# Kernel optimization log

Hardware: AMD Instinct MI355X
Metric: run time of the kernel (lower is better)

## Reference

```python
import jax, jax.numpy as jnp
import numpy as np

N = 8            # n_qubits
N_LAYERS_CRZ = 1

_H = jnp.array([[1.0, 1.0], [1.0, -1.0]], dtype=jnp.complex64) / np.sqrt(2).astype(np.float32)
_X2 = jnp.array([[0.0, 1.0], [1.0, 0.0]], dtype=jnp.complex64)
_I2 = jnp.eye(2, dtype=jnp.complex64)


def _apply_1q(state, U, q):
    # shared (2,2) gate on wire q; state: (B, 2,...,2)
    moved = jnp.moveaxis(state, 1 + q, -1)
    out = jnp.einsum('ij,...j->...i', U, moved)
    return jnp.moveaxis(out, -1, 1 + q)


def _apply_1q_batched(state, U, q):
    # per-sample (B,2,2) gate on wire q
    moved = jnp.moveaxis(state, 1 + q, -1)
    out = jnp.einsum('bij,b...j->b...i', U, moved)
    return jnp.moveaxis(out, -1, 1 + q)


def _apply_diag_batched(state, d, q):
    # per-sample diagonal (B,2) phases on wire q
    shape = (d.shape[0],) + (1,) * q + (2,) + (1,) * (N - 1 - q)
    return state * d.reshape(shape)


def _apply_ctrl_diag(state, ph, c, t):
    # controlled diagonal: apply phases ph (2,) on target t when control c == 1
    moved = jnp.moveaxis(state, (1 + c, 1 + t), (-2, -1))
    d = jnp.stack([jnp.ones(2, state.dtype), ph])  # (bc, bt)
    moved = moved * d
    return jnp.moveaxis(moved, (-2, -1), (1 + c, 1 + t))


def _apply_ctrl(state, U, c, t):
    # controlled (2,2) gate, control c, target t
    moved = jnp.moveaxis(state, (1 + c, 1 + t), (-2, -1))
    s0 = moved[..., 0, :]
    s1 = jnp.einsum('ij,...j->...i', U, moved[..., 1, :])
    out = jnp.stack([s0, s1], axis=-2)
    return jnp.moveaxis(out, (-2, -1), (1 + c, 1 + t))


def _circuit(X, weights):
    B = X.shape[0]
    state = jnp.zeros((B,) + (2,) * N, jnp.complex64)
    state = state.at[(slice(None),) + (0,) * N].set(1.0)

    # encoding: H, RZ(x[2q]), RY(x[2q+1]) on each wire q (2q+1 < 16 always)
    for q in range(N):
        state = _apply_1q(state, _H, q)
        th_z = X[:, 2 * q]
        d = jnp.stack([jnp.exp(-0.5j * th_z), jnp.exp(0.5j * th_z)], axis=-1)  # (B,2)
        state = _apply_diag_batched(state, d, q)
        half = 0.5 * X[:, 2 * q + 1]
        c, s = jnp.cos(half), jnp.sin(half)
        Ury = jnp.stack([jnp.stack([c, -s], -1), jnp.stack([s, c], -1)], -2)  # (B,2,2) real
        state = _apply_1q_batched(state, Ury, q)

    # CRZ ring
    for l in range(N_LAYERS_CRZ):
        for i in range(N):
            th = weights[l, i]
            ph = jnp.stack([jnp.exp(-0.5j * th), jnp.exp(0.5j * th)])
            state = _apply_ctrl_diag(state, ph, i, (i + 1) % N)

    # all-to-all CRX
    for i in range(N):
        for j in range(N):
            if j == i:
                continue
            half = 0.5 * weights[N_LAYERS_CRZ + i, j]
            Urx = jnp.cos(half) * _I2 + (-1j * jnp.sin(half)) * _X2
            state = _apply_ctrl(state, Urx, i, j)

    probs = jnp.real(state * jnp.conj(state)).reshape(B, 2 ** N)
    q_idx = jnp.arange(N)
    bits = (jnp.arange(2 ** N)[None, :] >> (N - 1 - q_idx)[:, None]) & 1  # (N, 2^N)
    signs = (1.0 - 2.0 * bits).astype(probs.dtype)
    return probs @ signs.T  # (B, N) <Z_q> expectations


def setup_inputs() -> dict:
    key = jax.random.key(0)
    k1, k2 = jax.random.split(key)
    X = jax.random.normal(k1, (16384, 2 * N), dtype=jnp.float32)
    weights = jax.random.normal(k2, (N_LAYERS_CRZ + N, (N_LAYERS_CRZ + N) * N), dtype=jnp.float32)
    return {"X": X, "weights": weights}


def reference(X, weights):
    return _circuit(X, weights)
```

## Files before the change

### kernel.cpp

```cpp
#include <hip/hip_runtime.h>


typedef _Float16 half_t;
typedef __attribute__((ext_vector_type(8))) _Float16 half8;
typedef __attribute__((ext_vector_type(4))) float float4v;

static __device__ __forceinline__ float rlane(float v, int src) {
    return __int_as_float(__builtin_amdgcn_readlane(__float_as_int(v), src));
}
template <int CTRL>
static __device__ __forceinline__ float dppf(float x) {
    return __int_as_float(__builtin_amdgcn_update_dpp(0, __float_as_int(x), CTRL, 0xF, 0xF, true));
}
static __device__ __forceinline__ float xor1f(float x) { return dppf<0xB1>(x); }
static __device__ __forceinline__ float xor2f(float x) { return dppf<0x4E>(x); }
static __device__ __forceinline__ float xor4f(float x) { return dppf<0x1B>(dppf<0x141>(x)); }
static __device__ __forceinline__ float xor8f(float x) { return dppf<0x128>(x); }
static __device__ __forceinline__ float xorMf(float x, int m) {
    if (m == 1) return xor1f(x);
    if (m == 2) return xor2f(x);
    if (m == 4) return xor4f(x);
    return xor8f(x);
}
static __device__ __forceinline__ float2 xorM2(float2 a, int m) {
    float2 t; t.x = xorMf(a.x, m); t.y = xorMf(a.y, m); return t;
}
static __device__ __forceinline__ float2 cmul(float2 a, float2 b) {
    float2 t;
    t.x = a.x * b.x - a.y * b.y;
    t.y = a.x * b.y + a.y * b.x;
    return t;
}
static __device__ __forceinline__ float2 rotA(float2 t, float2 u, float c, float s) {
    float2 d;
    d.x = c * t.x + s * u.y;
    d.y = c * t.y - s * u.x;
    return d;
}

__global__ __launch_bounds__(256, 4) void buildV_kernel(const float* __restrict__ W,
                                                        half_t* __restrict__ Vr,
                                                        half_t* __restrict__ Vi) {
    const int lane = threadIdx.x & 63;
    const int g = lane >> 4;
    const int s = lane & 15;
    const int eid = (blockIdx.x * 4 + (threadIdx.x >> 6)) * 4 + g;

    float gcv = 1.0f, gsv = 0.0f;
    if (lane < 56) {
        const int i = lane / 7;
        const int jj = lane - 7 * i;
        const int j = jj + (jj >= i ? 1 : 0);
        const float h = 0.5f * W[(1 + i) * 72 + j];
        __sincosf(h, &gsv, &gcv);
    }

    float2 a[16];
#pragma unroll
    for (int r = 0; r < 16; ++r) {
        a[r].x = (s == (eid & 15) && r == (eid >> 4)) ? 1.0f : 0.0f;
        a[r].y = 0.0f;
    }

    {
        const float wv0 = W[0], wv1 = W[1], wv2 = W[2], wv3 = W[3];
        const float wv4 = W[4], wv5 = W[5], wv6 = W[6], wv7 = W[7];
        const int s3 = (s >> 3) & 1, s2 = (s >> 2) & 1, s1 = (s >> 1) & 1, s0 = s & 1;
        float phiS = 0.0f;
        phiS += s3 ? (s2 ? wv4 : -wv4) : 0.0f;
        phiS += s2 ? (s1 ? wv5 : -wv5) : 0.0f;
        phiS += s1 ? (s0 ? wv6 : -wv6) : 0.0f;
        const float termA = s3 ? wv3 : -wv3;
        const float termB = s0 ? wv7 : 0.0f;
#pragma unroll
        for (int r = 0; r < 16; ++r) {
            const int b3 = (r >> 3) & 1, b2 = (r >> 2) & 1, b1 = (r >> 1) & 1, b0 = r & 1;
            float phi = phiS + (b3 ? termB : -termB);
            if (b3) phi += b2 ? wv0 : -wv0;
            if (b2) phi += b1 ? wv1 : -wv1;
            if (b1) phi += b0 ? wv2 : -wv2;
            if (b0) phi += termA;
            float2 ph;
            __sincosf(0.5f * phi, &ph.y, &ph.x);
            a[r] = cmul(a[r], ph);
        }
    }

#pragma unroll
    for (int i = 0; i < 4; ++i) {
        float cg[8], sg[8];
#pragma unroll
        for (int j = 0; j < 8; ++j) {
            if (j == i) continue;
            const int gi = i * 7 + (j < i ? j : j - 1);
            cg[j] = rlane(gcv, gi);
            sg[j] = rlane(gsv, gi);
        }
        const int rc = 3 - i;
#pragma unroll
        for (int j = 0; j < 8; ++j) {
            if (j == i) continue;
            if (j < 4) {
                const int mt = 1 << (3 - j);
#pragma unroll
                for (int r = 0; r < 16; ++r) {
                    if (!((r >> rc) & 1)) continue;
                    if (r & mt) continue;
                    const int rp = r | mt;
                    const float2 t = a[r], u = a[rp];
                    a[r]  = rotA(t, u, cg[j], sg[j]);
                    a[rp] = rotA(u, t, cg[j], sg[j]);
                }
            } else {
                const int ms = 1 << (7 - j);
#pragma unroll
                for (int r = 0; r < 16; ++r) {
                    if (!((r >> rc) & 1)) continue;
                    const float2 p = xorM2(a[r], ms);
                    a[r] = rotA(a[r], p, cg[j], sg[j]);
                }
            }
        }
    }

#pragma unroll
    for (int k = 1; k <= 8; k <<= 1) {
        const bool sk = (s & k) != 0;
#pragma unroll
        for (int r = 0; r < 16; ++r) {
            if (r & k) continue;
            const int rp = r | k;
            const float2 tp = xorM2(a[rp], k);
            const float2 tr = xorM2(a[r],  k);
            a[r].x  = sk ? tp.x : a[r].x;
            a[r].y  = sk ? tp.y : a[r].y;
            a[rp].x = sk ? a[rp].x : tr.x;
            a[rp].y = sk ? a[rp].y : tr.y;
        }
    }

#pragma unroll
    for (int i = 4; i < 8; ++i) {
        float cg[8], sg[8];
#pragma unroll
        for (int j = 0; j < 8; ++j) {
            if (j == i) continue;
            const int gi = i * 7 + (j < i ? j : j - 1);
            cg[j] = rlane(gcv, gi);
            sg[j] = rlane(gsv, gi);
        }
        const int rc = 7 - i;
#pragma unroll
        for (int j = 0; j < 8; ++j) {
            if (j == i) continue;
            if (j < 4) {
                const int ms = 1 << (3 - j);
#pragma unroll
                for (int r = 0; r < 16; ++r) {
                    if (!((r >> rc) & 1)) continue;
                    const float2 p = xorM2(a[r], ms);
                    a[r] = rotA(a[r], p, cg[j], sg[j]);
                }
            } else {
                const int mt = 1 << (7 - j);
#pragma unroll
                for (int r = 0; r < 16; ++r) {
                    if (!((r >> rc) & 1)) continue;
                    if (r & mt) continue;
                    const int rp = r | mt;
                    const float2 t = a[r], u = a[rp];
                    a[r]  = rotA(t, u, cg[j], sg[j]);
                    a[rp] = rotA(u, t, cg[j], sg[j]);
                }
            }
        }
    }

    const int ks = eid >> 5, kq = (eid >> 3) & 3, jj = eid & 7;
#pragma unroll
    for (int r = 0; r < 16; ++r) {
        const int off = ((s * 8 + ks) * 64 + kq * 16 + r) * 8 + jj;
        Vr[off] = (half_t)a[r].x;
        Vi[off] = (half_t)a[r].y;
    }
}

#define PSI_STRIDE 264

__global__ __launch_bounds__(256, 2) void gemm_kernel(const float* __restrict__ X,
                                                      const half_t* __restrict__ Vr,
                                                      const half_t* __restrict__ Vi,
                                                      float* __restrict__ out,
                                                      int B) {
    __shared__ float4 u_lds[32][8];
    __shared__ half_t psir[32][PSI_STRIDE];
    __shared__ half_t psii[32][PSI_STRIDE];
    __shared__ float part[32][8][4];

    const int tid = threadIdx.x;
    const int rowbase = blockIdx.x * 32;

    {
        const int m = tid >> 3, q = tid & 7;
        int row = rowbase + m; if (row >= B) row = B - 1;
        const float2 xq = ((const float2*)X)[row * 8 + q];
        float cz, sz, cy, sy;
        __sincosf(0.5f * xq.x, &sz, &cz);
        __sincosf(0.5f * xq.y, &sy, &cy);
        float4 u;
        u.x = (cy - sy) * cz;  u.y = -(cy + sy) * sz;
        u.z = (cy + sy) * cz;  u.w = (cy - sy) * sz;
        u_lds[m][q] = u;
    }
    __syncthreads();

    {
        const int m = tid >> 3, kh = tid & 7;
        float2 uu[8][2];
#pragma unroll
        for (int q = 0; q < 8; ++q) {
            const float4 u = u_lds[m][q];
            uu[q][0].x = u.x; uu[q][0].y = u.y;
            uu[q][1].x = u.z; uu[q][1].y = u.w;
        }
        const float2 pre = cmul(cmul(uu[0][(kh >> 2) & 1], uu[1][(kh >> 1) & 1]), uu[2][kh & 1]);
        float2 t1[2], t2[4], t3[8], t4[16];
        t1[0] = cmul(pre, uu[3][0]);  t1[1] = cmul(pre, uu[3][1]);
#pragma unroll
        for (int h = 0; h < 2; ++h) { t2[2*h] = cmul(t1[h], uu[4][0]); t2[2*h+1] = cmul(t1[h], uu[4][1]); }
#pragma unroll
        for (int h = 0; h < 4; ++h) { t3[2*h] = cmul(t2[h], uu[5][0]); t3[2*h+1] = cmul(t2[h], uu[5][1]); }
#pragma unroll
        for (int h = 0; h < 8; ++h) { t4[2*h] = cmul(t3[h], uu[6][0]); t4[2*h+1] = cmul(t3[h], uu[6][1]); }
        unsigned int* pr = (unsigned int*)&psir[m][kh * 32];
        unsigned int* pi = (unsigned int*)&psii[m][kh * 32];
#pragma unroll
        for (int h = 0; h < 16; ++h) {
            const float2 v0 = cmul(t4[h], uu[7][0]);
            const float2 v1 = cmul(t4[h], uu[7][1]);
            union { half_t h2[2]; unsigned int u; } cr, ci;
            cr.h2[0] = (half_t)v0.x; cr.h2[1] = (half_t)v1.x;
            ci.h2[0] = (half_t)v0.y; ci.h2[1] = (half_t)v1.y;
            pr[h] = cr.u; pi[h] = ci.u;
        }
    }
    __syncthreads();

    const int w = tid >> 6;
    const int lane = tid & 63;
    const int m16 = lane & 15;
    float4v Cr[2][4], Ci[2][4];
#pragma unroll
    for (int rt = 0; rt < 2; ++rt)
#pragma unroll
        for (int t = 0; t < 4; ++t) {
            Cr[rt][t] = (float4v){0.f, 0.f, 0.f, 0.f};
            Ci[rt][t] = (float4v){0.f, 0.f, 0.f, 0.f};
        }
#pragma unroll
    for (int ks = 0; ks < 8; ++ks) {
        const int koff = ks * 32 + (lane >> 4) * 8;
        const half8 Ar0 = *(const half8*)&psir[m16][koff];
        const half8 Ai0 = *(const half8*)&psii[m16][koff];
        const half8 Ar1 = *(const half8*)&psir[16 + m16][koff];
        const half8 Ai1 = *(const half8*)&psii[16 + m16][koff];
#pragma unroll
        for (int t = 0; t < 4; ++t) {
            const int T = w * 4 + t;
            const int boff = ((T * 8 + ks) * 64 + lane) * 8;
            const half8 Br = *(const half8*)(Vr + boff);
            const half8 Bi = *(const half8*)(Vi + boff);
            const half8 Bin = -Bi;
            Cr[0][t] = __builtin_amdgcn_mfma_f32_16x16x32_f16(Ar0, Br,  Cr[0][t], 0, 0, 0);
            Cr[0][t] = __builtin_amdgcn_mfma_f32_16x16x32_f16(Ai0, Bin, Cr[0][t], 0, 0, 0);
            Ci[0][t] = __builtin_amdgcn_mfma_f32_16x16x32_f16(Ar0, Bi,  Ci[0][t], 0, 0, 0);
            Ci[0][t] = __builtin_amdgcn_mfma_f32_16x16x32_f16(Ai0, Br,  Ci[0][t], 0, 0, 0);
            Cr[1][t] = __builtin_amdgcn_mfma_f32_16x16x32_f16(Ar1, Br,  Cr[1][t], 0, 0, 0);
            Cr[1][t] = __builtin_amdgcn_mfma_f32_16x16x32_f16(Ai1, Bin, Cr[1][t], 0, 0, 0);
            Ci[1][t] = __builtin_amdgcn_mfma_f32_16x16x32_f16(Ar1, Bi,  Ci[1][t], 0, 0, 0);
            Ci[1][t] = __builtin_amdgcn_mfma_f32_16x16x32_f16(Ai1, Br,  Ci[1][t], 0, 0, 0);
        }
    }

    const float sw0 = ((w >> 1) & 1) ? -1.0f : 1.0f;
    const float sw1 = (w & 1) ? -1.0f : 1.0f;
    const int quad = lane >> 4;
#pragma unroll
    for (int rt = 0; rt < 2; ++rt) {
        float A0[4] = {0.f, 0.f, 0.f, 0.f};
        float A2[4] = {0.f, 0.f, 0.f, 0.f};
        float A3[4] = {0.f, 0.f, 0.f, 0.f};
#pragma unroll
        for (int t = 0; t < 4; ++t) {
            const int T = w * 4 + t;
            const float s2 = ((T >> 1) & 1) ? -1.0f : 1.0f;
            const float s3 = (T & 1) ? -1.0f : 1.0f;
#pragma unroll
            for (int reg = 0; reg < 4; ++reg) {
                const float cr = Cr[rt][t][reg], ci = Ci[rt][t][reg];
                const float P = cr * cr + ci * ci;
                A0[reg] += P;
                A2[reg] += s2 * P;
                A3[reg] += s3 * P;
            }
        }
#pragma unroll
        for (int reg = 0; reg < 4; ++reg) {
            float Z = A0[reg], E7, E6, E5, E4;
            { const float tt = xor1f(Z); E7 = Z - tt; Z += tt; }
            { const float tt = xor2f(Z); E6 = Z - tt; Z += tt; E7 += xor2f(E7); }
            { const float tt = xor4f(Z); E5 = Z - tt; Z += tt; E7 += xor4f(E7); E6 += xor4f(E6); }
            { const float tt = xor8f(Z); E4 = Z - tt; Z += tt; E7 += xor8f(E7); E6 += xor8f(E6); E5 += xor8f(E5); }
            float Q2 = A2[reg]; Q2 += xor1f(Q2); Q2 += xor2f(Q2); Q2 += xor4f(Q2); Q2 += xor8f(Q2);
            float Q3 = A3[reg]; Q3 += xor1f(Q3); Q3 += xor2f(Q3); Q3 += xor4f(Q3); Q3 += xor8f(Q3);
            if (m16 == 0) {
                const int m = rt * 16 + quad * 4 + reg;
                part[m][0][w] = sw0 * Z;
                part[m][1][w] = sw1 * Z;
                part[m][2][w] = Q2;
                part[m][3][w] = Q3;
                part[m][4][w] = E4;
                part[m][5][w] = E5;
                part[m][6][w] = E6;
                part[m][7][w] = E7;
            }
        }
    }
    __syncthreads();
    {
        const int m = tid >> 3, q = tid & 7;
        const int row = rowbase + m;
        if (row < B) {
            const float v = part[m][q][0] + part[m][q][1] + part[m][q][2] + part[m][q][3];
            out[row * 8 + q] = v * (1.0f / 256.0f);
        }
    }
}

extern "C" void kernel_launch(void* const* d_in, const int* in_sizes, int n_in,
                              void* d_out, int out_size, void* d_ws, size_t ws_size,
                              hipStream_t stream) {
    const float* X = (const float*)d_in[0];
    const float* W = (const float*)d_in[1];
    float* out = (float*)d_out;
    const int B = in_sizes[0] / 16;
    half_t* Vr = (half_t*)d_ws;
    half_t* Vi = Vr + 256 * 256;
    buildV_kernel<<<16, 256, 0, stream>>>(W, Vr, Vi);
    gemm_kernel<<<(B + 31) / 32, 256, 0, stream>>>(X, Vr, Vi, out, B);
}
```

Before: 81.53 us.

## Fuse unitary build and GEMM into one kernel with a grid-wide atomic barrier

Merges the separate unitary-construction kernel and the batched GEMM kernel into one launch. The first 16 blocks build V and publish it with a threadfence, while all blocks prepare their per-row product states in LDS; then every block waits on a global atomic counter before reading V for the MFMA stage. The aim is to remove the inter-kernel gap and overlap V construction with the state preparation. In exchange it adds a memset launch for the counter and a spin barrier that relies on all 512 blocks being co-resident, which risks deadlock if occupancy drops. The order of two independent MFMA calls also changes.

```diff
diff --git a/kernel.cpp b/kernel.cpp
--- a/kernel.cpp
+++ b/kernel.cpp
@@ -38,167 +38,168 @@
     return d;
 }
 
-__global__ __launch_bounds__(256, 4) void buildV_kernel(const float* __restrict__ W,
-                                                        half_t* __restrict__ Vr,
-                                                        half_t* __restrict__ Vi) {
-    const int lane = threadIdx.x & 63;
-    const int g = lane >> 4;
-    const int s = lane & 15;
-    const int eid = (blockIdx.x * 4 + (threadIdx.x >> 6)) * 4 + g;
-
-    float gcv = 1.0f, gsv = 0.0f;
-    if (lane < 56) {
-        const int i = lane / 7;
-        const int jj = lane - 7 * i;
-        const int j = jj + (jj >= i ? 1 : 0);
-        const float h = 0.5f * W[(1 + i) * 72 + j];
-        __sincosf(h, &gsv, &gcv);
-    }
-
-    float2 a[16];
-#pragma unroll
-    for (int r = 0; r < 16; ++r) {
-        a[r].x = (s == (eid & 15) && r == (eid >> 4)) ? 1.0f : 0.0f;
-        a[r].y = 0.0f;
-    }
-
-    {
-        const float wv0 = W[0], wv1 = W[1], wv2 = W[2], wv3 = W[3];
-        const float wv4 = W[4], wv5 = W[5], wv6 = W[6], wv7 = W[7];
-        const int s3 = (s >> 3) & 1, s2 = (s >> 2) & 1, s1 = (s >> 1) & 1, s0 = s & 1;
-        float phiS = 0.0f;
-        phiS += s3 ? (s2 ? wv4 : -wv4) : 0.0f;
-        phiS += s2 ? (s1 ? wv5 : -wv5) : 0.0f;
-        phiS += s1 ? (s0 ? wv6 : -wv6) : 0.0f;
-        const float termA = s3 ? wv3 : -wv3;
-        const float termB = s0 ? wv7 : 0.0f;
-#pragma unroll
-        for (int r = 0; r < 16; ++r) {
-            const int b3 = (r >> 3) & 1, b2 = (r >> 2) & 1, b1 = (r >> 1) & 1, b0 = r & 1;
-            float phi = phiS + (b3 ? termB : -termB);
-            if (b3) phi += b2 ? wv0 : -wv0;
-            if (b2) phi += b1 ? wv1 : -wv1;
-            if (b1) phi += b0 ? wv2 : -wv2;
-            if (b0) phi += termA;
-            float2 ph;
-            __sincosf(0.5f * phi, &ph.y, &ph.x);
-            a[r] = cmul(a[r], ph);
-        }
-    }
-
-#pragma unroll
-    for (int i = 0; i < 4; ++i) {
-        float cg[8], sg[8];
-#pragma unroll
-        for (int j = 0; j < 8; ++j) {
-            if (j == i) continue;
-            const int gi = i * 7 + (j < i ? j : j - 1);
-            cg[j] = rlane(gcv, gi);
-            sg[j] = rlane(gsv, gi);
-        }
-        const int rc = 3 - i;
-#pragma unroll
-        for (int j = 0; j < 8; ++j) {
-            if (j == i) continue;
-            if (j < 4) {
-                const int mt = 1 << (3 - j);
-#pragma unroll
-                for (int r = 0; r < 16; ++r) {
-                    if (!((r >> rc) & 1)) continue;
-                    if (r & mt) continue;
-                    const int rp = r | mt;
-                    const float2 t = a[r], u = a[rp];
-                    a[r]  = rotA(t, u, cg[j], sg[j]);
-                    a[rp] = rotA(u, t, cg[j], sg[j]);
-                }
-            } else {
-                const int ms = 1 << (7 - j);
-#pragma unroll
-                for (int r = 0; r < 16; ++r) {
-                    if (!((r >> rc) & 1)) continue;
-                    const float2 p = xorM2(a[r], ms);
-                    a[r] = rotA(a[r], p, cg[j], sg[j]);
-                }
-            }
-        }
-    }
-
-#pragma unroll
-    for (int k = 1; k <= 8; k <<= 1) {
-        const bool sk = (s & k) != 0;
-#pragma unroll
-        for (int r = 0; r < 16; ++r) {
-            if (r & k) continue;
-            const int rp = r | k;
-            const float2 tp = xorM2(a[rp], k);
-            const float2 tr = xorM2(a[r],  k);
-            a[r].x  = sk ? tp.x : a[r].x;
-            a[r].y  = sk ? tp.y : a[r].y;
-            a[rp].x = sk ? a[rp].x : tr.x;
-            a[rp].y = sk ? a[rp].y : tr.y;
-        }
-    }
-
-#pragma unroll
-    for (int i = 4; i < 8; ++i) {
-        float cg[8], sg[8];
-#pragma unroll
-        for (int j = 0; j < 8; ++j) {
-            if (j == i) continue;
-            const int gi = i * 7 + (j < i ? j : j - 1);
-            cg[j] = rlane(gcv, gi);
-            sg[j] = rlane(gsv, gi);
-        }
-        const int rc = 7 - i;
-#pragma unroll
-        for (int j = 0; j < 8; ++j) {
-            if (j == i) continue;
-            if (j < 4) {
-                const int ms = 1 << (3 - j);
-#pragma unroll
-                for (int r = 0; r < 16; ++r) {
-                    if (!((r >> rc) & 1)) continue;
-                    const float2 p = xorM2(a[r], ms);
-                    a[r] = rotA(a[r], p, cg[j], sg[j]);
-                }
-            } else {
-                const int mt = 1 << (7 - j);
-#pragma unroll
-                for (int r = 0; r < 16; ++r) {
-                    if (!((r >> rc) & 1)) continue;
-                    if (r & mt) continue;
-                    const int rp = r | mt;
-                    const float2 t = a[r], u = a[rp];
-                    a[r]  = rotA(t, u, cg[j], sg[j]);
-                    a[rp] = rotA(u, t, cg[j], sg[j]);
-                }
-            }
-        }
-    }
-
-    const int ks = eid >> 5, kq = (eid >> 3) & 3, jj = eid & 7;
-#pragma unroll
-    for (int r = 0; r < 16; ++r) {
-        const int off = ((s * 8 + ks) * 64 + kq * 16 + r) * 8 + jj;
-        Vr[off] = (half_t)a[r].x;
-        Vi[off] = (half_t)a[r].y;
-    }
-}
-
 #define PSI_STRIDE 264
 
-__global__ __launch_bounds__(256, 2) void gemm_kernel(const float* __restrict__ X,
-                                                      const half_t* __restrict__ Vr,
-                                                      const half_t* __restrict__ Vi,
-                                                      float* __restrict__ out,
-                                                      int B) {
+__global__ __launch_bounds__(256, 2) void fused_kernel(const float* __restrict__ X,
+                                                       const float* __restrict__ W,
+                                                       float* __restrict__ out,
+                                                       half_t* __restrict__ Vr,
+                                                       half_t* __restrict__ Vi,
+                                                       unsigned int* __restrict__ cnt,
+                                                       int B, unsigned int nblk) {
     __shared__ float4 u_lds[32][8];
     __shared__ half_t psir[32][PSI_STRIDE];
     __shared__ half_t psii[32][PSI_STRIDE];
     __shared__ float part[32][8][4];
 
     const int tid = threadIdx.x;
+    const int lane = tid & 63;
     const int rowbase = blockIdx.x * 32;
+
+    if (blockIdx.x < 16) {
+        const int g = lane >> 4;
+        const int s = lane & 15;
+        const int eid = (blockIdx.x * 4 + (tid >> 6)) * 4 + g;
+
+        float gcv = 1.0f, gsv = 0.0f;
+        if (lane < 56) {
+            const int i = lane / 7;
+            const int jj = lane - 7 * i;
+            const int j = jj + (jj >= i ? 1 : 0);
+            const float h = 0.5f * W[(1 + i) * 72 + j];
+            __sincosf(h, &gsv, &gcv);
+        }
+
+        float2 a[16];
+#pragma unroll
+        for (int r = 0; r < 16; ++r) {
+            a[r].x = (s == (eid & 15) && r == (eid >> 4)) ? 1.0f : 0.0f;
+            a[r].y = 0.0f;
+        }
+
+        {
+            const float wv0 = W[0], wv1 = W[1], wv2 = W[2], wv3 = W[3];
+            const float wv4 = W[4], wv5 = W[5], wv6 = W[6], wv7 = W[7];
+            const int s3 = (s >> 3) & 1, s2 = (s >> 2) & 1, s1 = (s >> 1) & 1, s0 = s & 1;
+            float phiS = 0.0f;
+            phiS += s3 ? (s2 ? wv4 : -wv4) : 0.0f;
+            phiS += s2 ? (s1 ? wv5 : -wv5) : 0.0f;
+            phiS += s1 ? (s0 ? wv6 : -wv6) : 0.0f;
+            const float termA = s3 ? wv3 : -wv3;
+            const float termB = s0 ? wv7 : 0.0f;
+#pragma unroll
+            for (int r = 0; r < 16; ++r) {
+                const int b3 = (r >> 3) & 1, b2 = (r >> 2) & 1, b1 = (r >> 1) & 1, b0 = r & 1;
+                float phi = phiS + (b3 ? termB : -termB);
+                if (b3) phi += b2 ? wv0 : -wv0;
+                if (b2) phi += b1 ? wv1 : -wv1;
+                if (b1) phi += b0 ? wv2 : -wv2;
+                if (b0) phi += termA;
+                float2 ph;
+                __sincosf(0.5f * phi, &ph.y, &ph.x);
+                a[r] = cmul(a[r], ph);
+            }
+        }
+
+#pragma unroll
+        for (int i = 0; i < 4; ++i) {
+            float cg[8], sg[8];
+#pragma unroll
+            for (int j = 0; j < 8; ++j) {
+                if (j == i) continue;
+                const int gi = i * 7 + (j < i ? j : j - 1);
+                cg[j] = rlane(gcv, gi);
+                sg[j] = rlane(gsv, gi);
+            }
+            const int rc = 3 - i;
+#pragma unroll
+            for (int j = 0; j < 8; ++j) {
+                if (j == i) continue;
+                if (j < 4) {
+                    const int mt = 1 << (3 - j);
+#pragma unroll
+                    for (int r = 0; r < 16; ++r) {
+                        if (!((r >> rc) & 1)) continue;
+                        if (r & mt) continue;
+                        const int rp = r | mt;
+                        const float2 t = a[r], u = a[rp];
+                        a[r]  = rotA(t, u, cg[j], sg[j]);
+                        a[rp] = rotA(u, t, cg[j], sg[j]);
+                    }
+                } else {
+                    const int ms = 1 << (7 - j);
+#pragma unroll
+                    for (int r = 0; r < 16; ++r) {
+                        if (!((r >> rc) & 1)) continue;
+                        const float2 p = xorM2(a[r], ms);
+                        a[r] = rotA(a[r], p, cg[j], sg[j]);
+                    }
+                }
+            }
+        }
+
+#pragma unroll
+        for (int k = 1; k <= 8; k <<= 1) {
+            const bool sk = (s & k) != 0;
+#pragma unroll
+            for (int r = 0; r < 16; ++r) {
+                if (r & k) continue;
+                const int rp = r | k;
+                const float2 tp = xorM2(a[rp], k);
+                const float2 tr = xorM2(a[r],  k);
+                a[r].x  = sk ? tp.x : a[r].x;
+                a[r].y  = sk ? tp.y : a[r].y;
+                a[rp].x = sk ? a[rp].x : tr.x;
+                a[rp].y = sk ? a[rp].y : tr.y;
+            }
+        }
+
+#pragma unroll
+        for (int i = 4; i < 8; ++i) {
+            float cg[8], sg[8];
+#pragma unroll
+            for (int j = 0; j < 8; ++j) {
+                if (j == i) continue;
+                const int gi = i * 7 + (j < i ? j : j - 1);
+                cg[j] = rlane(gcv, gi);
+                sg[j] = rlane(gsv, gi);
+            }
+            const int rc = 7 - i;
+#pragma unroll
+            for (int j = 0; j < 8; ++j) {
+                if (j == i) continue;
+                if (j < 4) {
+                    const int ms = 1 << (3 - j);
+#pragma unroll
+                    for (int r = 0; r < 16; ++r) {
+                        if (!((r >> rc) & 1)) continue;
+                        const float2 p = xorM2(a[r], ms);
+                        a[r] = rotA(a[r], p, cg[j], sg[j]);
+                    }
+                } else {
+                    const int mt = 1 << (7 - j);
+#pragma unroll
+                    for (int r = 0; r < 16; ++r) {
+                        if (!((r >> rc) & 1)) continue;
+                        if (r & mt) continue;
+                        const int rp = r | mt;
+                        const float2 t = a[r], u = a[rp];
+                        a[r]  = rotA(t, u, cg[j], sg[j]);
+                        a[rp] = rotA(u, t, cg[j], sg[j]);
+                    }
+                }
+            }
+        }
+
+        const int ks = eid >> 5, kq = (eid >> 3) & 3, jj = eid & 7;
+#pragma unroll
+        for (int r = 0; r < 16; ++r) {
+            const int off = ((s * 8 + ks) * 64 + kq * 16 + r) * 8 + jj;
+            Vr[off] = (half_t)a[r].x;
+            Vi[off] = (half_t)a[r].y;
+        }
+        __threadfence();
+    }
 
     {
         const int m = tid >> 3, q = tid & 7;
@@ -213,7 +214,6 @@
         u_lds[m][q] = u;
     }
     __syncthreads();
-
     {
         const int m = tid >> 3, kh = tid & 7;
         float2 uu[8][2];
@@ -246,8 +246,16 @@
     }
     __syncthreads();
 
+    if (tid == 0) {
+        __hip_atomic_fetch_add(cnt, 1u, __ATOMIC_RELEASE, __HIP_MEMORY_SCOPE_AGENT);
+        while (__hip_atomic_load(cnt, __ATOMIC_RELAXED, __HIP_MEMORY_SCOPE_AGENT) < nblk) {
+            __builtin_amdgcn_s_sleep(2);
+        }
+    }
+    __syncthreads();
+    __builtin_amdgcn_fence(__ATOMIC_ACQUIRE, "agent");
+
     const int w = tid >> 6;
-    const int lane = tid & 63;
     const int m16 = lane & 15;
     float4v Cr[2][4], Ci[2][4];
 #pragma unroll
@@ -277,8 +285,8 @@
             Ci[0][t] = __builtin_amdgcn_mfma_f32_16x16x32_f16(Ai0, Br,  Ci[0][t], 0, 0, 0);
             Cr[1][t] = __builtin_amdgcn_mfma_f32_16x16x32_f16(Ar1, Br,  Cr[1][t], 0, 0, 0);
             Cr[1][t] = __builtin_amdgcn_mfma_f32_16x16x32_f16(Ai1, Bin, Cr[1][t], 0, 0, 0);
+            Ci[1][t] = __builtin_amdgcn_mfma_f32_16x16x32_f16(Ai1, Br,  Ci[1][t], 0, 0, 0);
             Ci[1][t] = __builtin_amdgcn_mfma_f32_16x16x32_f16(Ar1, Bi,  Ci[1][t], 0, 0, 0);
-            Ci[1][t] = __builtin_amdgcn_mfma_f32_16x16x32_f16(Ai1, Br,  Ci[1][t], 0, 0, 0);
         }
     }
 
@@ -346,6 +354,8 @@
     const int B = in_sizes[0] / 16;
     half_t* Vr = (half_t*)d_ws;
     half_t* Vi = Vr + 256 * 256;
-    buildV_kernel<<<16, 256, 0, stream>>>(W, Vr, Vi);
-    gemm_kernel<<<(B + 31) / 32, 256, 0, stream>>>(X, Vr, Vi, out, B);
-}
+    unsigned int* cnt = (unsigned int*)((char*)d_ws + (1 << 20));
+    const unsigned int blocks = (unsigned int)((B + 31) / 32);
+    hipMemsetAsync(cnt, 0, 4, stream);
+    fused_kernel<<<blocks, 256, 0, stream>>>(X, W, out, Vr, Vi, cnt, B, blocks);
+}
```

Measured after the change: 116.1 us. 1.42x slower.
